# Kernel tuning notes

Hardware: AMD Instinct MI355X
Metric: run time of the kernel (lower is better)

Reference implementation:

```python
import jax, jax.numpy as jnp
import numpy as np

N = 20000      # nodes
E = 640000     # edges (avg degree 32)
F = 128        # hidden_channels == num_filters
RBF = 64       # num_rbf
H = 8          # num_heads
DH = F // H    # head dim
T = 5          # number of distinct element types present in z
CUT = 5.0      # cutoff_upper (cutoff_lower = 0)


def setup_inputs() -> dict:
    key = jax.random.key(0)
    ks = jax.random.split(key, 20)
    s = 0.05
    inp = {
        "x": jax.random.normal(ks[0], (N, F), jnp.float32),
        "z": jax.random.randint(ks[1], (N,), 0, T, jnp.int32),
        "edge_index": jax.random.randint(ks[2], (2, E), 0, N, jnp.int32),
        "edge_weight": jax.random.uniform(ks[3], (E,), jnp.float32) * CUT,
        "edge_attr": jax.random.normal(ks[4], (E, RBF), jnp.float32),
        # ElemConv params
        "lin1_w": jax.random.normal(ks[5], (F, F), jnp.float32) / np.sqrt(F),
        "f_w1": jax.random.normal(ks[6], (F, RBF), jnp.float32) / np.sqrt(RBF),
        "f_b1": jnp.zeros((F,), jnp.float32),
        "f_w2": jax.random.normal(ks[7], (F, F), jnp.float32) / np.sqrt(F),
        "f_b2": jnp.zeros((F,), jnp.float32),
        # ElemAttn params
        "q_w": jax.random.normal(ks[8], (F, F), jnp.float32) / np.sqrt(F),
        "q_b": jax.random.normal(ks[9], (F,), jnp.float32) * s,
        "k_w": jax.random.normal(ks[10], (F, F), jnp.float32) / np.sqrt(F),
        "k_b": jax.random.normal(ks[11], (F,), jnp.float32) * s,
        "v_w": jax.random.normal(ks[12], (F, F), jnp.float32) / np.sqrt(F),
        "v_b": jax.random.normal(ks[13], (F,), jnp.float32) * s,
        "o1_w": jax.random.normal(ks[14], (F, F), jnp.float32) / np.sqrt(F),
        "o1_b": jax.random.normal(ks[15], (F,), jnp.float32) * s,
        "o2_w": jax.random.normal(ks[16], (F, F), jnp.float32) / np.sqrt(F),
        "o2_b": jax.random.normal(ks[17], (F,), jnp.float32) * s,
    }
    return inp


def reference(x, z, edge_index, edge_weight, edge_attr,
              lin1_w, f_w1, f_b1, f_w2, f_b2,
              q_w, q_b, k_w, k_b, v_w, v_b, o1_w, o1_b, o2_w, o2_b):
    silu = jax.nn.silu
    src, dst = edge_index[0], edge_index[1]

    # ---- ElemConv ----
    # CosineCutoff (cutoff_lower = 0)
    C = 0.5 * (jnp.cos(edge_weight * (jnp.pi / CUT)) + 1.0)
    C = C * (edge_weight < CUT).astype(x.dtype)
    # filter_net(edge_attr) * C
    W = silu(edge_attr @ f_w1.T + f_b1) @ f_w2.T + f_b2          # [E, F]
    W = W * C[:, None]
    xl = x @ lin1_w.T                                             # [N, F]
    msg = xl[src] * W                                             # [E, F]
    # aggregate by unique (z_j, dst) pair == dense [N, T] slot grid
    seg = dst * T + z[src]                                        # [E]
    y = jax.ops.segment_sum(msg, seg, num_segments=N * T).reshape(N, T, F)
    cnt = jax.ops.segment_sum(jnp.ones((E,), x.dtype), seg, num_segments=N * T)
    pm = (cnt > 0).astype(x.dtype).reshape(N, T)                  # presence mask

    # ---- ElemAttn (block-diagonal per target node over present slots) ----
    q = (y @ q_w.T + q_b).reshape(N, T, H, DH)
    k = (y @ k_w.T + k_b).reshape(N, T, H, DH)
    v = (y @ v_w.T + v_b).reshape(N, T, H, DH)
    attn = silu(jnp.einsum('nihd,njhd->nhij', q, k))              # [N, H, T, T]
    attn = attn * (pm[:, None, :, None] * pm[:, None, None, :])
    out = jnp.einsum('nhij,njhd->nihd', attn, v).reshape(N, T, F)
    out = out @ o1_w.T + o1_b                                     # [N, T, F]
    node = jnp.einsum('ntf,nt->nf', out, pm)                      # scatter-add by node
    return silu(node @ o2_w.T + o2_b)                             # [N, F]
```

## Files before the change

### kernel.cpp

```cpp
#include <hip/hip_runtime.h>

#define N_NODES 20000
#define E_EDGES 640000
#define F_DIM 128
#define RBF_DIM 64
#define T_TYPES 5
#define NSEG (N_NODES * T_TYPES)
#define EPB 128
#define MTS 136

typedef __attribute__((ext_vector_type(8))) short short8;
typedef __attribute__((ext_vector_type(4))) float f32x4;

__device__ __forceinline__ float silu_f(float x) { return x / (1.0f + __expf(-x)); }

__device__ __forceinline__ ushort f2bf(float f) {
  unsigned u = __float_as_uint(f);
  u += 0x7fffu + ((u >> 16) & 1u);
  return (ushort)(u >> 16);
}
__device__ __forceinline__ float bf2f(ushort u) {
  return __uint_as_float(((unsigned)u) << 16);
}
__device__ __forceinline__ unsigned cvt_pk(float lo, float hi) {
  unsigned r;
  asm("v_cvt_pk_bf16_f32 %0, %1, %2" : "=v"(r) : "v"(lo), "v"(hi));
  return r;
}
union S8U4 {
  short8 s;
  unsigned u[4];
};

__global__ __launch_bounds__(256) void prep_kernel(
    const float* __restrict__ w1, const float* __restrict__ w2,
    const float* __restrict__ qw, const float* __restrict__ kw,
    const float* __restrict__ vw, const float* __restrict__ o1w,
    const float* __restrict__ o2w, const float* __restrict__ lw,
    ushort* __restrict__ w1b, ushort* __restrict__ w2b,
    ushort* __restrict__ qwb, ushort* __restrict__ kwb,
    ushort* __restrict__ vwb, ushort* __restrict__ o1wb,
    ushort* __restrict__ o2wb, ushort* __restrict__ lwb,
    int* __restrict__ hist) {
  int i = blockIdx.x * 256 + threadIdx.x;
  if (i < F_DIM * RBF_DIM) w1b[i] = f2bf(w1[i]);
  if (i < F_DIM * F_DIM) {
    w2b[i] = f2bf(w2[i]);
    qwb[i] = f2bf(qw[i]);
    kwb[i] = f2bf(kw[i]);
    vwb[i] = f2bf(vw[i]);
    o1wb[i] = f2bf(o1w[i]);
    o2wb[i] = f2bf(o2w[i]);
    lwb[i] = f2bf(lw[i]);
  }
  for (int j = i; j < NSEG; j += 64 * 256) hist[j] = 0;
}

__global__ __launch_bounds__(256) void stage1_kernel(
    const int* __restrict__ srcp, const int* __restrict__ dstp,
    const int* __restrict__ z, int* __restrict__ hist, int* __restrict__ rnk,
    float* __restrict__ y, const float* __restrict__ x,
    const ushort* __restrict__ lwb, ushort* __restrict__ xlb) {
  const int b = blockIdx.x;
  const int tid = threadIdx.x;
  if (b < E_EDGES / 256) {
    int e = b * 256 + tid;
    int s = srcp[e];
    int seg = dstp[e] * T_TYPES + z[s];
    rnk[e] = atomicAdd(&hist[seg], 1);
    float4* yz = (float4*)(y + (size_t)b * 5120);
#pragma unroll
    for (int i = 0; i < 5; ++i)
      yz[tid + i * 256] = make_float4(0.f, 0.f, 0.f, 0.f);
  } else {
    const int lane = tid & 63;
    const int w = tid >> 6;
    const int lr = lane & 15, lh = lane >> 4;
    const int r0 = (b - E_EDGES / 256) * 80;

    f32x4 acc[5][2] = {};
#pragma unroll
    for (int ksi = 0; ksi < 4; ++ksi) {
      short8 B[2];
#pragma unroll
      for (int fc = 0; fc < 2; ++fc)
        B[fc] = *(const short8*)(lwb + (size_t)(w * 32 + fc * 16 + lr) * 128 +
                                 ksi * 32 + lh * 8);
#pragma unroll
      for (int fm = 0; fm < 5; ++fm) {
        const float* ap =
            x + (size_t)(r0 + fm * 16 + lr) * 128 + ksi * 32 + lh * 8;
        float4 a0 = *(const float4*)ap;
        float4 a1 = *(const float4*)(ap + 4);
        S8U4 t;
        t.u[0] = cvt_pk(a0.x, a0.y);
        t.u[1] = cvt_pk(a0.z, a0.w);
        t.u[2] = cvt_pk(a1.x, a1.y);
        t.u[3] = cvt_pk(a1.z, a1.w);
#pragma unroll
        for (int fc = 0; fc < 2; ++fc)
          acc[fm][fc] = __builtin_amdgcn_mfma_f32_16x16x32_bf16(
              t.s, B[fc], acc[fm][fc], 0, 0, 0);
      }
    }
#pragma unroll
    for (int fm = 0; fm < 5; ++fm)
#pragma unroll
      for (int fc = 0; fc < 2; ++fc)
#pragma unroll
        for (int rp = 0; rp < 4; rp += 2) {
          int rrow = fm * 16 + lh * 4 + rp;
          int col = w * 32 + fc * 16 + lr;
          unsigned u = cvt_pk(acc[fm][fc][rp], acc[fm][fc][rp + 1]);
          xlb[(size_t)(r0 + rrow) * 128 + col] = (ushort)u;
          xlb[(size_t)(r0 + rrow + 1) * 128 + col] = (ushort)(u >> 16);
        }
  }
}

__global__ __launch_bounds__(256) void scan1_kernel(const int* __restrict__ hist,
                                                    int* __restrict__ offs,
                                                    int* __restrict__ bsums) {
  __shared__ int lds[256];
  int tid = threadIdx.x;
  int base = blockIdx.x * 1024 + tid * 4;
  int v[4];
  int s = 0;
#pragma unroll
  for (int i = 0; i < 4; ++i) {
    v[i] = (base + i < NSEG) ? hist[base + i] : 0;
    s += v[i];
  }
  lds[tid] = s;
  __syncthreads();
  for (int d = 1; d < 256; d <<= 1) {
    int t = (tid >= d) ? lds[tid - d] : 0;
    __syncthreads();
    lds[tid] += t;
    __syncthreads();
  }
  int excl = lds[tid] - s;
#pragma unroll
  for (int i = 0; i < 4; ++i) {
    if (base + i < NSEG) offs[base + i] = excl;
    excl += v[i];
  }
  if (tid == 255) bsums[blockIdx.x] = lds[255];
}

__global__ __launch_bounds__(256) void scatter_kernel(
    const int* __restrict__ srcp, const int* __restrict__ dstp,
    const int* __restrict__ z, const float* __restrict__ ewp,
    const int* __restrict__ offs, const int* __restrict__ bsums,
    const int* __restrict__ rnk, int* __restrict__ perm,
    int* __restrict__ ssegS, int* __restrict__ srcS,
    float* __restrict__ sCS) {
  __shared__ int pb[128];
  const int tid = threadIdx.x;
  const int NB_SCAN = (NSEG + 1023) / 1024;
  if (tid < 128) pb[tid] = (tid < NB_SCAN) ? bsums[tid] : 0;
  __syncthreads();
  int vown = (tid < 128) ? pb[tid] : 0;
  for (int d = 1; d < 128; d <<= 1) {
    int t = (tid >= d && tid < 128) ? pb[tid - d] : 0;
    __syncthreads();
    if (tid < 128) pb[tid] += t;
    __syncthreads();
  }
  if (tid < 128) pb[tid] -= vown;
  __syncthreads();

  int e = blockIdx.x * 256 + tid;
  int s = srcp[e];
  int seg = dstp[e] * T_TYPES + z[s];
  int pos = offs[seg] + pb[seg >> 10] + rnk[e];
  perm[pos] = e;
  ssegS[pos] = seg;
  srcS[pos] = s * 128;
  float wd = ewp[e];
  float c = 0.5f * (__cosf(wd * 0.6283185307179586f) + 1.0f);
  sCS[pos] = (wd < 5.0f) ? c : 0.0f;
}

__global__ __launch_bounds__(256, 4) void edge_mfma_kernel(
    const float* __restrict__ edge_attr, const int* __restrict__ perm,
    const int* __restrict__ ssegS, const int* __restrict__ srcS,
    const float* __restrict__ sCS, const ushort* __restrict__ w1b,
    const float* __restrict__ b1, const ushort* __restrict__ w2b,
    const float* __restrict__ b2, const ushort* __restrict__ xlb,
    float* __restrict__ y) {
  __shared__ ushort hs[128 * MTS];
  __shared__ float sC[EPB];
  __shared__ int srcoff[EPB];
  __shared__ int sseg[EPB];
  __shared__ unsigned long long smask[2];

  const int tid = threadIdx.x;
  const int e0 = blockIdx.x * EPB;
  const int lane = tid & 63;
  const int w = tid >> 6;
  const int wm = w >> 1, wn = w & 1;
  const int lr = lane & 15, lh = lane >> 4;

  int prow[4];
#pragma unroll
  for (int fm = 0; fm < 4; ++fm) prow[fm] = perm[e0 + wm * 64 + fm * 16 + lr];

  float rb1[4], rb2[4];
#pragma unroll
  for (int fc = 0; fc < 4; ++fc) {
    int n = wn * 64 + fc * 16 + lr;
    rb1[fc] = b1[n];
    rb2[fc] = b2[n];
  }

  if (tid < EPB) {
    int p = e0 + tid;
    srcoff[tid] = srcS[p];
    sseg[tid] = ssegS[p];
    sC[tid] = sCS[p];
  }

  f32x4 acc[4][4] = {};
#pragma unroll
  for (int ks = 0; ks < 2; ++ks) {
    const int k0 = ks * 32;
    short8 af[4], bfr[4];
#pragma unroll
    for (int fm = 0; fm < 4; ++fm) {
      const float* ap = edge_attr + (size_t)prow[fm] * 64 + k0 + lh * 8;
      float4 a0 = *(const float4*)ap;
      float4 a1 = *(const float4*)(ap + 4);
      S8U4 t;
      t.u[0] = cvt_pk(a0.x, a0.y);
      t.u[1] = cvt_pk(a0.z, a0.w);
      t.u[2] = cvt_pk(a1.x, a1.y);
      t.u[3] = cvt_pk(a1.z, a1.w);
      af[fm] = t.s;
    }
#pragma unroll
    for (int fc = 0; fc < 4; ++fc)
      bfr[fc] = *(const short8*)(w1b + (size_t)(wn * 64 + fc * 16 + lr) * 64 +
                                 k0 + lh * 8);
#pragma unroll
    for (int fm = 0; fm < 4; ++fm)
#pragma unroll
      for (int fc = 0; fc < 4; ++fc)
        acc[fm][fc] = __builtin_amdgcn_mfma_f32_16x16x32_bf16(
            af[fm], bfr[fc], acc[fm][fc], 0, 0, 0);
  }

#pragma unroll
  for (int fm = 0; fm < 4; ++fm) {
#pragma unroll
    for (int fc = 0; fc < 4; ++fc) {
#pragma unroll
      for (int rp = 0; rp < 4; rp += 2) {
        int ml0 = wm * 64 + fm * 16 + lh * 4 + rp;
        int ml1 = ml0 + 1;
        int n = wn * 64 + fc * 16 + lr;
        float h0 = silu_f(acc[fm][fc][rp] + rb1[fc]);
        float h1 = silu_f(acc[fm][fc][rp + 1] + rb1[fc]);
        unsigned u = cvt_pk(h0, h1);
        hs[(ml0 * 256 + ((n * 2) ^ ((ml0 & 7) << 4))) >> 1] = (ushort)u;
        hs[(ml1 * 256 + ((n * 2) ^ ((ml1 & 7) << 4))) >> 1] = (ushort)(u >> 16);
      }
    }
  }
  __syncthreads();

  if (tid < EPB) {
    int head = (tid == 0) || (sseg[tid] != sseg[tid - 1]);
    unsigned long long m = __ballot(head);
    if ((tid & 63) == 0) smask[tid >> 6] = m;
  }

  f32x4 acc2[4][4] = {};
#pragma unroll
  for (int ks = 0; ks < 4; ++ks) {
    const int k0 = ks * 32;
    short8 af[4], bfr[4];
#pragma unroll
    for (int fm = 0; fm < 4; ++fm) {
      int ml = wm * 64 + fm * 16 + lr;
      int byte_in_row = (k0 * 2 + lh * 16) ^ ((ml & 7) << 4);
      af[fm] = *(const short8*)&hs[(ml * 256 + byte_in_row) >> 1];
    }
#pragma unroll
    for (int fc = 0; fc < 4; ++fc)
      bfr[fc] = *(const short8*)(w2b + (size_t)(wn * 64 + fc * 16 + lr) * 128 +
                                 k0 + lh * 8);
#pragma unroll
    for (int fm = 0; fm < 4; ++fm)
#pragma unroll
      for (int fc = 0; fc < 4; ++fc)
        acc2[fm][fc] = __builtin_amdgcn_mfma_f32_16x16x32_bf16(
            af[fm], bfr[fc], acc2[fm][fc], 0, 0, 0);
  }
  __syncthreads();

#pragma unroll
  for (int fm = 0; fm < 4; ++fm) {
#pragma unroll
    for (int rp = 0; rp < 4; rp += 2) {
      int ml0 = wm * 64 + fm * 16 + lh * 4 + rp;
      float c0 = sC[ml0], c1 = sC[ml0 + 1];
#pragma unroll
      for (int fc = 0; fc < 4; ++fc) {
        int n = wn * 64 + fc * 16 + lr;
        float v0 = (acc2[fm][fc][rp] + rb2[fc]) * c0;
        float v1 = (acc2[fm][fc][rp + 1] + rb2[fc]) * c1;
        *(unsigned*)&hs[n * MTS + ml0] = cvt_pk(v0, v1);
      }
    }
  }
  __syncthreads();

  {
    int cp = tid & 63;
    int q = tid >> 6;
    int rbase = q * 32;
    int c0 = cp * 2;
    unsigned mm = (unsigned)(smask[q >> 1] >> ((q & 1) * 32));
    float a0 = 0.0f, a1 = 0.0f;
    int cur = sseg[rbase];
    bool first = true;
#pragma unroll
    for (int it = 0; it < 4; ++it) {
      int r0 = rbase + it * 8;
      short8 m0 = *(const short8*)&hs[c0 * MTS + r0];
      short8 m1 = *(const short8*)&hs[(c0 + 1) * MTS + r0];
      unsigned xv[8];
#pragma unroll
      for (int j = 0; j < 8; ++j)
        xv[j] = *(const unsigned*)&xlb[(size_t)srcoff[r0 + j] + c0];
#pragma unroll
      for (int j = 0; j < 8; ++j) {
        int rr = it * 8 + j;
        if (rr && ((mm >> rr) & 1u)) {
          float* yp = &y[(size_t)cur * 128 + c0];
          if (first) {
            atomicAdd(yp, a0);
            atomicAdd(yp + 1, a1);
            first = false;
          } else {
            yp[0] = a0;
            yp[1] = a1;
          }
          a0 = a1 = 0.0f;
          cur = sseg[r0 + j];
        }
        a0 += bf2f((ushort)m0[j]) * bf2f((ushort)xv[j]);
        a1 += bf2f((ushort)m1[j]) * bf2f((ushort)(xv[j] >> 16));
      }
    }
    float* yp = &y[(size_t)cur * 128 + c0];
    atomicAdd(yp, a0);
    atomicAdd(yp + 1, a1);
  }
}

#define QS 136
#define NB 16
__global__ __launch_bounds__(256) void attn_out_kernel(
    const float* __restrict__ y, const int* __restrict__ hist,
    const ushort* __restrict__ qwb, const ushort* __restrict__ kwb,
    const ushort* __restrict__ vwb, const float* __restrict__ qb,
    const float* __restrict__ kb, const float* __restrict__ vb,
    const ushort* __restrict__ o1wb, const float* __restrict__ o1b,
    const ushort* __restrict__ o2wb, const float* __restrict__ o2b,
    float* __restrict__ outp) {
  __shared__ ushort bufA[80 * QS];
  __shared__ ushort bufB[80 * QS];
  __shared__ float aap[NB * 8 * 2 * 5];
  __shared__ float pmv[80];
  __shared__ float snpm[NB];
  __shared__ float sxb[3][128];

  const int tid = threadIdx.x;
  const int xcd = blockIdx.x & 7;
  const int loc = blockIdx.x >> 3;
  const int bid = (xcd < 2 ? xcd * 157 : 314 + (xcd - 2) * 156) + loc;
  const int n0 = bid * NB;
  const int row0 = n0 * T_TYPES;
  const int lane = tid & 63;
  const int w = tid >> 6;
  const int lr = lane & 15, lh = lane >> 4;

  if (tid < 128) {
    sxb[0][tid] = qb[tid];
    sxb[1][tid] = kb[tid];
    sxb[2][tid] = vb[tid];
  }
  if (tid < 80) pmv[tid] = (hist[(size_t)row0 + tid] > 0) ? 1.0f : 0.0f;

  short8 A[4][5];
#pragma unroll
  for (int ksi = 0; ksi < 4; ++ksi) {
#pragma unroll
    for (int fm = 0; fm < 5; ++fm) {
      const float* ap =
          y + (size_t)(row0 + fm * 16 + lr) * 128 + ksi * 32 + lh * 8;
      float4 a0 = *(const float4*)ap;
      float4 a1 = *(const float4*)(ap + 4);
      S8U4 t;
      t.u[0] = cvt_pk(a0.x, a0.y);
      t.u[1] = cvt_pk(a0.z, a0.w);
      t.u[2] = cvt_pk(a1.x, a1.y);
      t.u[3] = cvt_pk(a1.z, a1.w);
      A[ksi][fm] = t.s;
    }
  }
  __syncthreads();
  if (tid < NB) {
    float s = 0.0f;
#pragma unroll
    for (int t = 0; t < 5; ++t) s += pmv[tid * 5 + t];
    snpm[tid] = s;
  }

  auto do_proj = [&](const ushort* __restrict__ Wb, const float* bias_row,
                     ushort* __restrict__ dst) {
    f32x4 acc[5][2] = {};
#pragma unroll
    for (int ksi = 0; ksi < 4; ++ksi) {
      short8 B[2];
#pragma unroll
      for (int fc = 0; fc < 2; ++fc)
        B[fc] = *(const short8*)(Wb + (size_t)(w * 32 + fc * 16 + lr) * 128 +
                                 ksi * 32 + lh * 8);
#pragma unroll
      for (int fm = 0; fm < 5; ++fm)
#pragma unroll
        for (int fc = 0; fc < 2; ++fc)
          acc[fm][fc] = __builtin_amdgcn_mfma_f32_16x16x32_bf16(
              A[ksi][fm], B[fc], acc[fm][fc], 0, 0, 0);
    }
#pragma unroll
    for (int fm = 0; fm < 5; ++fm)
#pragma unroll
      for (int fc = 0; fc < 2; ++fc)
#pragma unroll
        for (int rp = 0; rp < 4; rp += 2) {
          int rrow = fm * 16 + lh * 4 + rp;
          int col = w * 32 + fc * 16 + lr;
          float v0 = acc[fm][fc][rp] + bias_row[col];
          float v1 = acc[fm][fc][rp + 1] + bias_row[col];
          unsigned u = cvt_pk(v0, v1);
          dst[rrow * QS + col] = (ushort)u;
          dst[(rrow + 1) * QS + col] = (ushort)(u >> 16);
        }
  };

  do_proj(qwb, sxb[0], bufA);
  do_proj(kwb, sxb[1], bufB);
  __syncthreads();

  {
    int n = tid >> 4, h = (tid >> 1) & 7, g = tid & 1;
    int i0 = g ? 3 : 0;
    int cnt = g ? 2 : 3;
    float kv[5][16];
#pragma unroll
    for (int j = 0; j < 5; ++j) {
      short8 v0 = *(const short8*)&bufB[(n * 5 + j) * QS + h * 16];
      short8 v1 = *(const short8*)&bufB[(n * 5 + j) * QS + h * 16 + 8];
#pragma unroll
      for (int d = 0; d < 8; ++d) {
        kv[j][d] = bf2f((ushort)v0[d]);
        kv[j][d + 8] = bf2f((ushort)v1[d]);
      }
    }
    float a[5] = {};
    for (int ii = 0; ii < cnt; ++ii) {
      int i = i0 + ii;
      float qv[16];
      short8 q0 = *(const short8*)&bufA[(n * 5 + i) * QS + h * 16];
      short8 q1 = *(const short8*)&bufA[(n * 5 + i) * QS + h * 16 + 8];
#pragma unroll
      for (int d = 0; d < 8; ++d) {
        qv[d] = bf2f((ushort)q0[d]);
        qv[d + 8] = bf2f((ushort)q1[d]);
      }
      float pmi = pmv[n * 5 + i];
#pragma unroll
      for (int j = 0; j < 5; ++j) {
        float dd = 0.0f;
#pragma unroll
        for (int d = 0; d < 16; ++d) dd += qv[d] * kv[j][d];
        a[j] += pmi * silu_f(dd);
      }
    }
#pragma unroll
    for (int j = 0; j < 5; ++j) aap[((n * 8 + h) * 2 + g) * 5 + j] = a[j];
  }
  __syncthreads();

  do_proj(vwb, sxb[2], bufA);
  __syncthreads();

  {
    int n = tid >> 4;
    int o = tid & 15;
    int f0 = o * 8;
    int h = f0 >> 4;
    float acc8[8] = {};
#pragma unroll
    for (int j = 0; j < 5; ++j) {
      float a = (aap[((n * 8 + h) * 2 + 0) * 5 + j] +
                 aap[((n * 8 + h) * 2 + 1) * 5 + j]) *
                pmv[n * 5 + j];
      short8 vv8 = *(const short8*)&bufA[(n * 5 + j) * QS + f0];
#pragma unroll
      for (int d = 0; d < 8; ++d) acc8[d] += a * bf2f((ushort)vv8[d]);
    }
    S8U4 t;
    t.u[0] = cvt_pk(acc8[0], acc8[1]);
    t.u[1] = cvt_pk(acc8[2], acc8[3]);
    t.u[2] = cvt_pk(acc8[4], acc8[5]);
    t.u[3] = cvt_pk(acc8[6], acc8[7]);
    *(short8*)&bufB[n * QS + f0] = t.s;
  }
  __syncthreads();

  {
    f32x4 acc[2] = {};
#pragma unroll
    for (int ksi = 0; ksi < 4; ++ksi) {
      short8 af = *(const short8*)&bufB[lr * QS + ksi * 32 + lh * 8];
      short8 B0 = *(const short8*)(o1wb + (size_t)(w * 32 + lr) * 128 +
                                   ksi * 32 + lh * 8);
      short8 B1 = *(const short8*)(o1wb + (size_t)(w * 32 + 16 + lr) * 128 +
                                   ksi * 32 + lh * 8);
      acc[0] = __builtin_amdgcn_mfma_f32_16x16x32_bf16(af, B0, acc[0], 0, 0, 0);
      acc[1] = __builtin_amdgcn_mfma_f32_16x16x32_bf16(af, B1, acc[1], 0, 0, 0);
    }
#pragma unroll
    for (int fc = 0; fc < 2; ++fc) {
      int col = w * 32 + fc * 16 + lr;
      float bb = o1b[col];
#pragma unroll
      for (int r = 0; r < 4; ++r) {
        int row = lh * 4 + r;
        bufA[row * QS + col] = f2bf(acc[fc][r] + snpm[row] * bb);
      }
    }
  }
  __syncthreads();

  {
    f32x4 acc[2] = {};
#pragma unroll
    for (int ksi = 0; ksi < 4; ++ksi) {
      short8 af = *(const short8*)&bufA[lr * QS + ksi * 32 + lh * 8];
      short8 B0 = *(const short8*)(o2wb + (size_t)(w * 32 + lr) * 128 +
                                   ksi * 32 + lh * 8);
      short8 B1 = *(const short8*)(o2wb + (size_t)(w * 32 + 16 + lr) * 128 +
                                   ksi * 32 + lh * 8);
      acc[0] = __builtin_amdgcn_mfma_f32_16x16x32_bf16(af, B0, acc[0], 0, 0, 0);
      acc[1] = __builtin_amdgcn_mfma_f32_16x16x32_bf16(af, B1, acc[1], 0, 0, 0);
    }
#pragma unroll
    for (int fc = 0; fc < 2; ++fc) {
      int col = w * 32 + fc * 16 + lr;
      float bb = o2b[col];
#pragma unroll
      for (int r = 0; r < 4; ++r) {
        int row = lh * 4 + r;
        outp[(size_t)(n0 + row) * 128 + col] = silu_f(acc[fc][r] + bb);
      }
    }
  }
}

extern "C" void kernel_launch(void* const* d_in, const int* in_sizes, int n_in,
                              void* d_out, int out_size, void* d_ws, size_t ws_size,
                              hipStream_t stream) {
  const float* x = (const float*)d_in[0];
  const int* z = (const int*)d_in[1];
  const int* ei = (const int*)d_in[2];
  const float* ew = (const float*)d_in[3];
  const float* ea = (const float*)d_in[4];
  const float* lin1_w = (const float*)d_in[5];
  const float* fw1 = (const float*)d_in[6];
  const float* fb1 = (const float*)d_in[7];
  const float* fw2 = (const float*)d_in[8];
  const float* fb2 = (const float*)d_in[9];
  const float* qw = (const float*)d_in[10];
  const float* qb = (const float*)d_in[11];
  const float* kw = (const float*)d_in[12];
  const float* kb = (const float*)d_in[13];
  const float* vw = (const float*)d_in[14];
  const float* vb = (const float*)d_in[15];
  const float* o1w = (const float*)d_in[16];
  const float* o1b = (const float*)d_in[17];
  const float* o2w = (const float*)d_in[18];
  const float* o2b = (const float*)d_in[19];
  float* outp = (float*)d_out;
  float* ws = (float*)d_ws;

  float* y = ws;
  ushort* xlb = (ushort*)(y + (size_t)NSEG * F_DIM);
  ushort* w1b = xlb + (size_t)N_NODES * F_DIM;
  ushort* w2b = w1b + F_DIM * RBF_DIM;
  ushort* qwb = w2b + F_DIM * F_DIM;
  ushort* kwb = qwb + F_DIM * F_DIM;
  ushort* vwb = kwb + F_DIM * F_DIM;
  ushort* o1wb = vwb + F_DIM * F_DIM;
  ushort* o2wb = o1wb + F_DIM * F_DIM;
  ushort* lwb = o2wb + F_DIM * F_DIM;
  int* hist = (int*)(lwb + F_DIM * F_DIM);
  int* offs = hist + NSEG;
  int* bsums = offs + NSEG;
  int* rnk = bsums + 128;
  int* perm = rnk + E_EDGES;
  int* ssegS = perm + E_EDGES;
  int* srcS = ssegS + E_EDGES;
  float* sCS = (float*)(srcS + E_EDGES);

  const int* srcp = ei;
  const int* dstp = ei + E_EDGES;
  const int NB_SCAN = (NSEG + 1023) / 1024;

  prep_kernel<<<64, 256, 0, stream>>>(fw1, fw2, qw, kw, vw, o1w, o2w, lin1_w,
                                      w1b, w2b, qwb, kwb, vwb, o1wb, o2wb, lwb,
                                      hist);
  stage1_kernel<<<E_EDGES / 256 + N_NODES / 80, 256, 0, stream>>>(
      srcp, dstp, z, hist, rnk, y, x, lwb, xlb);
  scan1_kernel<<<NB_SCAN, 256, 0, stream>>>(hist, offs, bsums);
  scatter_kernel<<<E_EDGES / 256, 256, 0, stream>>>(
      srcp, dstp, z, ew, offs, bsums, rnk, perm, ssegS, srcS, sCS);
  edge_mfma_kernel<<<E_EDGES / EPB, 256, 0, stream>>>(
      ea, perm, ssegS, srcS, sCS, w1b, fb1, w2b, fb2, xlb, y);
  attn_out_kernel<<<N_NODES / NB, 256, 0, stream>>>(y, hist, qwb, kwb, vwb, qb,
                                                    kb, vb, o1wb, o1b, o2wb,
                                                    o2b, outp);
}
```

Before: 291.6 us.

## Process two edge tiles per block and prefetch second tile's edge_attr early

Each edge_mfma block now handles 256 edges as two 128-edge tiles. The second tile's edge_attr rows are loaded into registers before the first tile's work begins, so the gather latency overlaps the first tile's GEMMs and scatter. This costs extra registers for the prefetched data, so the occupancy hint drops from 4 to 3 blocks per CU. The grid is halved to match.

```diff
diff --git a/kernel.cpp b/kernel.cpp
--- a/kernel.cpp
+++ b/kernel.cpp
@@ -182,7 +182,7 @@
   sCS[pos] = (wd < 5.0f) ? c : 0.0f;
 }
 
-__global__ __launch_bounds__(256, 4) void edge_mfma_kernel(
+__global__ __launch_bounds__(256, 3) void edge_mfma_kernel(
     const float* __restrict__ edge_attr, const int* __restrict__ perm,
     const int* __restrict__ ssegS, const int* __restrict__ srcS,
     const float* __restrict__ sCS, const ushort* __restrict__ w1b,
@@ -190,21 +190,31 @@
     const float* __restrict__ b2, const ushort* __restrict__ xlb,
     float* __restrict__ y) {
   __shared__ ushort hs[128 * MTS];
-  __shared__ float sC[EPB];
-  __shared__ int srcoff[EPB];
-  __shared__ int sseg[EPB];
+  __shared__ float sC[256];
+  __shared__ int srcoff[256];
+  __shared__ int sseg[256];
   __shared__ unsigned long long smask[2];
 
   const int tid = threadIdx.x;
-  const int e0 = blockIdx.x * EPB;
+  const int e0 = blockIdx.x * 256;
   const int lane = tid & 63;
   const int w = tid >> 6;
   const int wm = w >> 1, wn = w & 1;
   const int lr = lane & 15, lh = lane >> 4;
 
-  int prow[4];
-#pragma unroll
-  for (int fm = 0; fm < 4; ++fm) prow[fm] = perm[e0 + wm * 64 + fm * 16 + lr];
+  {
+    int p = e0 + tid;
+    srcoff[tid] = srcS[p];
+    sseg[tid] = ssegS[p];
+    sC[tid] = sCS[p];
+  }
+
+  int prowA[4], prowB[4];
+#pragma unroll
+  for (int fm = 0; fm < 4; ++fm) {
+    prowA[fm] = perm[e0 + wm * 64 + fm * 16 + lr];
+    prowB[fm] = perm[e0 + 128 + wm * 64 + fm * 16 + lr];
+  }
 
   float rb1[4], rb2[4];
 #pragma unroll
@@ -214,21 +224,12 @@
     rb2[fc] = b2[n];
   }
 
-  if (tid < EPB) {
-    int p = e0 + tid;
-    srcoff[tid] = srcS[p];
-    sseg[tid] = ssegS[p];
-    sC[tid] = sCS[p];
-  }
-
-  f32x4 acc[4][4] = {};
-#pragma unroll
-  for (int ks = 0; ks < 2; ++ks) {
-    const int k0 = ks * 32;
-    short8 af[4], bfr[4];
+  short8 af0[2][4];
+#pragma unroll
+  for (int ks = 0; ks < 2; ++ks)
 #pragma unroll
     for (int fm = 0; fm < 4; ++fm) {
-      const float* ap = edge_attr + (size_t)prow[fm] * 64 + k0 + lh * 8;
+      const float* ap = edge_attr + (size_t)prowA[fm] * 64 + ks * 32 + lh * 8;
       float4 a0 = *(const float4*)ap;
       float4 a1 = *(const float4*)(ap + 4);
       S8U4 t;
@@ -236,128 +237,170 @@
       t.u[1] = cvt_pk(a0.z, a0.w);
       t.u[2] = cvt_pk(a1.x, a1.y);
       t.u[3] = cvt_pk(a1.z, a1.w);
-      af[fm] = t.s;
-    }
-#pragma unroll
-    for (int fc = 0; fc < 4; ++fc)
-      bfr[fc] = *(const short8*)(w1b + (size_t)(wn * 64 + fc * 16 + lr) * 64 +
-                                 k0 + lh * 8);
-#pragma unroll
-    for (int fm = 0; fm < 4; ++fm)
+      af0[ks][fm] = t.s;
+    }
+
+  float4 rB[2][4][2];
+#pragma unroll
+  for (int ks = 0; ks < 2; ++ks)
+#pragma unroll
+    for (int fm = 0; fm < 4; ++fm) {
+      const float* ap = edge_attr + (size_t)prowB[fm] * 64 + ks * 32 + lh * 8;
+      rB[ks][fm][0] = *(const float4*)ap;
+      rB[ks][fm][1] = *(const float4*)(ap + 4);
+    }
+
+  auto gemm1 = [&](const short8 (&af)[2][4], f32x4 (&acc)[4][4]) {
+#pragma unroll
+    for (int ks = 0; ks < 2; ++ks) {
+      short8 bfr[4];
 #pragma unroll
       for (int fc = 0; fc < 4; ++fc)
-        acc[fm][fc] = __builtin_amdgcn_mfma_f32_16x16x32_bf16(
-            af[fm], bfr[fc], acc[fm][fc], 0, 0, 0);
-  }
-
-#pragma unroll
-  for (int fm = 0; fm < 4; ++fm) {
-#pragma unroll
-    for (int fc = 0; fc < 4; ++fc) {
+        bfr[fc] = *(const short8*)(w1b + (size_t)(wn * 64 + fc * 16 + lr) * 64 +
+                                   ks * 32 + lh * 8);
+#pragma unroll
+      for (int fm = 0; fm < 4; ++fm)
+#pragma unroll
+        for (int fc = 0; fc < 4; ++fc)
+          acc[fm][fc] = __builtin_amdgcn_mfma_f32_16x16x32_bf16(
+              af[ks][fm], bfr[fc], acc[fm][fc], 0, 0, 0);
+    }
+  };
+
+  f32x4 acc0[4][4] = {};
+  gemm1(af0, acc0);
+
+  short8 afB[2][4];
+#pragma unroll
+  for (int ks = 0; ks < 2; ++ks)
+#pragma unroll
+    for (int fm = 0; fm < 4; ++fm) {
+      S8U4 t;
+      t.u[0] = cvt_pk(rB[ks][fm][0].x, rB[ks][fm][0].y);
+      t.u[1] = cvt_pk(rB[ks][fm][0].z, rB[ks][fm][0].w);
+      t.u[2] = cvt_pk(rB[ks][fm][1].x, rB[ks][fm][1].y);
+      t.u[3] = cvt_pk(rB[ks][fm][1].z, rB[ks][fm][1].w);
+      afB[ks][fm] = t.s;
+    }
+
+  auto rest = [&](f32x4 (&a)[4][4], int tb) {
+    __syncthreads();
+
+    if (tid < EPB) {
+      int head = (tid == 0) || (sseg[tb + tid] != sseg[tb + tid - 1]);
+      unsigned long long m = __ballot(head);
+      if ((tid & 63) == 0) smask[tid >> 6] = m;
+    }
+
+#pragma unroll
+    for (int fm = 0; fm < 4; ++fm) {
+#pragma unroll
+      for (int fc = 0; fc < 4; ++fc) {
+#pragma unroll
+        for (int rp = 0; rp < 4; rp += 2) {
+          int ml0 = wm * 64 + fm * 16 + lh * 4 + rp;
+          int ml1 = ml0 + 1;
+          int n = wn * 64 + fc * 16 + lr;
+          float h0 = silu_f(a[fm][fc][rp] + rb1[fc]);
+          float h1 = silu_f(a[fm][fc][rp + 1] + rb1[fc]);
+          unsigned u = cvt_pk(h0, h1);
+          hs[(ml0 * 256 + ((n * 2) ^ ((ml0 & 7) << 4))) >> 1] = (ushort)u;
+          hs[(ml1 * 256 + ((n * 2) ^ ((ml1 & 7) << 4))) >> 1] = (ushort)(u >> 16);
+        }
+      }
+    }
+    __syncthreads();
+
+    f32x4 acc2[4][4] = {};
+#pragma unroll
+    for (int ks = 0; ks < 4; ++ks) {
+      const int k0 = ks * 32;
+      short8 af[4], bfr[4];
+#pragma unroll
+      for (int fm = 0; fm < 4; ++fm) {
+        int ml = wm * 64 + fm * 16 + lr;
+        int byte_in_row = (k0 * 2 + lh * 16) ^ ((ml & 7) << 4);
+        af[fm] = *(const short8*)&hs[(ml * 256 + byte_in_row) >> 1];
+      }
+#pragma unroll
+      for (int fc = 0; fc < 4; ++fc)
+        bfr[fc] = *(const short8*)(w2b + (size_t)(wn * 64 + fc * 16 + lr) * 128 +
+                                   k0 + lh * 8);
+#pragma unroll
+      for (int fm = 0; fm < 4; ++fm)
+#pragma unroll
+        for (int fc = 0; fc < 4; ++fc)
+          acc2[fm][fc] = __builtin_amdgcn_mfma_f32_16x16x32_bf16(
+              af[fm], bfr[fc], acc2[fm][fc], 0, 0, 0);
+    }
+    __syncthreads();
+
+#pragma unroll
+    for (int fm = 0; fm < 4; ++fm) {
 #pragma unroll
       for (int rp = 0; rp < 4; rp += 2) {
         int ml0 = wm * 64 + fm * 16 + lh * 4 + rp;
-        int ml1 = ml0 + 1;
-        int n = wn * 64 + fc * 16 + lr;
-        float h0 = silu_f(acc[fm][fc][rp] + rb1[fc]);
-        float h1 = silu_f(acc[fm][fc][rp + 1] + rb1[fc]);
-        unsigned u = cvt_pk(h0, h1);
-        hs[(ml0 * 256 + ((n * 2) ^ ((ml0 & 7) << 4))) >> 1] = (ushort)u;
-        hs[(ml1 * 256 + ((n * 2) ^ ((ml1 & 7) << 4))) >> 1] = (ushort)(u >> 16);
-      }
-    }
-  }
-  __syncthreads();
-
-  if (tid < EPB) {
-    int head = (tid == 0) || (sseg[tid] != sseg[tid - 1]);
-    unsigned long long m = __ballot(head);
-    if ((tid & 63) == 0) smask[tid >> 6] = m;
-  }
-
-  f32x4 acc2[4][4] = {};
-#pragma unroll
-  for (int ks = 0; ks < 4; ++ks) {
-    const int k0 = ks * 32;
-    short8 af[4], bfr[4];
-#pragma unroll
-    for (int fm = 0; fm < 4; ++fm) {
-      int ml = wm * 64 + fm * 16 + lr;
-      int byte_in_row = (k0 * 2 + lh * 16) ^ ((ml & 7) << 4);
-      af[fm] = *(const short8*)&hs[(ml * 256 + byte_in_row) >> 1];
-    }
-#pragma unroll
-    for (int fc = 0; fc < 4; ++fc)
-      bfr[fc] = *(const short8*)(w2b + (size_t)(wn * 64 + fc * 16 + lr) * 128 +
-                                 k0 + lh * 8);
-#pragma unroll
-    for (int fm = 0; fm < 4; ++fm)
-#pragma unroll
-      for (int fc = 0; fc < 4; ++fc)
-        acc2[fm][fc] = __builtin_amdgcn_mfma_f32_16x16x32_bf16(
-            af[fm], bfr[fc], acc2[fm][fc], 0, 0, 0);
-  }
-  __syncthreads();
-
-#pragma unroll
-  for (int fm = 0; fm < 4; ++fm) {
-#pragma unroll
-    for (int rp = 0; rp < 4; rp += 2) {
-      int ml0 = wm * 64 + fm * 16 + lh * 4 + rp;
-      float c0 = sC[ml0], c1 = sC[ml0 + 1];
-#pragma unroll
-      for (int fc = 0; fc < 4; ++fc) {
-        int n = wn * 64 + fc * 16 + lr;
-        float v0 = (acc2[fm][fc][rp] + rb2[fc]) * c0;
-        float v1 = (acc2[fm][fc][rp + 1] + rb2[fc]) * c1;
-        *(unsigned*)&hs[n * MTS + ml0] = cvt_pk(v0, v1);
-      }
-    }
-  }
-  __syncthreads();
-
-  {
-    int cp = tid & 63;
-    int q = tid >> 6;
-    int rbase = q * 32;
-    int c0 = cp * 2;
-    unsigned mm = (unsigned)(smask[q >> 1] >> ((q & 1) * 32));
-    float a0 = 0.0f, a1 = 0.0f;
-    int cur = sseg[rbase];
-    bool first = true;
-#pragma unroll
-    for (int it = 0; it < 4; ++it) {
-      int r0 = rbase + it * 8;
-      short8 m0 = *(const short8*)&hs[c0 * MTS + r0];
-      short8 m1 = *(const short8*)&hs[(c0 + 1) * MTS + r0];
-      unsigned xv[8];
-#pragma unroll
-      for (int j = 0; j < 8; ++j)
-        xv[j] = *(const unsigned*)&xlb[(size_t)srcoff[r0 + j] + c0];
-#pragma unroll
-      for (int j = 0; j < 8; ++j) {
-        int rr = it * 8 + j;
-        if (rr && ((mm >> rr) & 1u)) {
-          float* yp = &y[(size_t)cur * 128 + c0];
-          if (first) {
-            atomicAdd(yp, a0);
-            atomicAdd(yp + 1, a1);
-            first = false;
-          } else {
-            yp[0] = a0;
-            yp[1] = a1;
+        float c0 = sC[tb + ml0], c1 = sC[tb + ml0 + 1];
+#pragma unroll
+        for (int fc = 0; fc < 4; ++fc) {
+          int n = wn * 64 + fc * 16 + lr;
+          float v0 = (acc2[fm][fc][rp] + rb2[fc]) * c0;
+          float v1 = (acc2[fm][fc][rp + 1] + rb2[fc]) * c1;
+          *(unsigned*)&hs[n * MTS + ml0] = cvt_pk(v0, v1);
+        }
+      }
+    }
+    __syncthreads();
+
+    {
+      int cp = tid & 63;
+      int q = tid >> 6;
+      int rbase = q * 32;
+      int c0 = cp * 2;
+      unsigned mm = (unsigned)(smask[q >> 1] >> ((q & 1) * 32));
+      float a0 = 0.0f, a1 = 0.0f;
+      int cur = sseg[tb + rbase];
+      bool first = true;
+#pragma unroll
+      for (int it = 0; it < 4; ++it) {
+        int r0 = rbase + it * 8;
+        short8 m0 = *(const short8*)&hs[c0 * MTS + r0];
+        short8 m1 = *(const short8*)&hs[(c0 + 1) * MTS + r0];
+        unsigned xv[8];
+#pragma unroll
+        for (int j = 0; j < 8; ++j)
+          xv[j] = *(const unsigned*)&xlb[(size_t)srcoff[tb + r0 + j] + c0];
+#pragma unroll
+        for (int j = 0; j < 8; ++j) {
+          int rr = it * 8 + j;
+          if (rr && ((mm >> rr) & 1u)) {
+            float* yp = &y[(size_t)cur * 128 + c0];
+            if (first) {
+              atomicAdd(yp, a0);
+              atomicAdd(yp + 1, a1);
+              first = false;
+            } else {
+              yp[0] = a0;
+              yp[1] = a1;
+            }
+            a0 = a1 = 0.0f;
+            cur = sseg[tb + r0 + j];
           }
-          a0 = a1 = 0.0f;
-          cur = sseg[r0 + j];
+          a0 += bf2f((ushort)m0[j]) * bf2f((ushort)xv[j]);
+          a1 += bf2f((ushort)m1[j]) * bf2f((ushort)(xv[j] >> 16));
         }
-        a0 += bf2f((ushort)m0[j]) * bf2f((ushort)xv[j]);
-        a1 += bf2f((ushort)m1[j]) * bf2f((ushort)(xv[j] >> 16));
-      }
-    }
-    float* yp = &y[(size_t)cur * 128 + c0];
-    atomicAdd(yp, a0);
-    atomicAdd(yp + 1, a1);
-  }
+      }
+      float* yp = &y[(size_t)cur * 128 + c0];
+      atomicAdd(yp, a0);
+      atomicAdd(yp + 1, a1);
+    }
+  };
+
+  rest(acc0, 0);
+
+  f32x4 acc1[4][4] = {};
+  gemm1(afB, acc1);
+  rest(acc1, 128);
 }
 
 #define QS 136
@@ -630,7 +673,7 @@
   scan1_kernel<<<NB_SCAN, 256, 0, stream>>>(hist, offs, bsums);
   scatter_kernel<<<E_EDGES / 256, 256, 0, stream>>>(
       srcp, dstp, z, ew, offs, bsums, rnk, perm, ssegS, srcS, sCS);
-  edge_mfma_kernel<<<E_EDGES / EPB, 256, 0, stream>>>(
+  edge_mfma_kernel<<<E_EDGES / 256, 256, 0, stream>>>(
       ea, perm, ssegS, srcS, sCS, w1b, fb1, w2b, fb2, xlb, y);
   attn_out_kernel<<<N_NODES / NB, 256, 0, stream>>>(y, hist, qwb, kwb, vwb, qb,
                                                     kb, vb, o1wb, o1b, o2wb,
```

Measured after the change: 374.8 us. 28.5% more time.
